# Kernel tuning notes

Measured on AMD Instinct MI355X. Metric: run time of the kernel, lower is better.

## Reference

```python
import jax, jax.numpy as jnp
import numpy as np

NEG_BIG = -9.0e15  # matches torch's -9000000000000000.0 mask fill
ALPHA = 0.2        # leakyrelu negative slope


def setup_inputs() -> dict:
    key = jax.random.key(0)
    k1, k2, k3, k4, k5 = jax.random.split(key, 5)
    N, F_in, F_out = 4096, 512, 64
    stdv = 1.0 / np.sqrt(F_out)
    x = jax.random.normal(k1, (N, F_in), dtype=jnp.float32)
    adj = jax.random.randint(k2, (N, N), 0, 2, dtype=jnp.int32)
    W = jax.random.uniform(k3, (F_in, F_out), dtype=jnp.float32, minval=-stdv, maxval=stdv)
    a = jax.random.normal(k4, (2 * F_out, 1), dtype=jnp.float32) * 0.1
    bias = jax.random.uniform(k5, (F_out,), dtype=jnp.float32, minval=-stdv, maxval=stdv)
    return {"x": x, "adj": adj, "W": W, "a": a, "bias": bias}


def _gat_forward(x, adj, W, a, bias):
    N = x.shape[0]
    F_out = W.shape[1]
    h = x @ W  # (N, F)
    a1 = a[:F_out, 0]   # weights hitting the first concat half
    a2 = a[F_out:, 0]   # weights hitting the second concat half
    # First half: row k=i*N+j of the concat holds h_j  ->  e1[j] = h_j . a1
    e1 = h @ a1  # (N,)
    # Second half of this repo's concat is NOT h_i; exact index algebra:
    # second[k=i*N+j, r] = h[(r*N+i)//F, (((r*N+i)%F)*N + j) % F]
    # Since it depends on j only via j % F, build table T[i, t] (t = j % F).
    r = jnp.arange(F_out)[:, None]          # (F, 1)
    i = jnp.arange(N)[None, :]              # (1, N)
    m = r * N + i                           # (F, N)
    p = m // F_out                          # row index into h
    s0 = m % F_out
    t = jnp.arange(F_out)                   # (F,)
    col = (s0[..., None] * N + t) % F_out   # (F, N, F) column index into h
    vals = h[p[..., None], col]             # (F, N, F)
    T = jnp.einsum('r,rit->it', a2, vals)   # (N, F)
    j = jnp.arange(N)
    e2 = T[:, j % F_out]                    # (N, N) second-half contribution
    e = e1[None, :] + e2                    # (N, N) pre-activation scores
    e = jnp.where(e > 0, e, ALPHA * e)      # LeakyReLU(0.2)
    e = jnp.where(adj > 0, e, NEG_BIG)      # mask non-edges
    att = jax.nn.softmax(e, axis=1)         # row-wise softmax (dropout = eval identity)
    out = jax.nn.relu(att @ h) + bias       # relu BEFORE bias add, as in source
    return out


def reference(x, adj, W, a, bias):
    return _gat_forward(x, adj, W, a, bias)
```

## Files before the change

kernel.cpp:

```cpp
#include <hip/hip_runtime.h>
#include <math.h>

#define N_NODES 4096
#define F_IN    512
#define F_OUT   64
#define ALPHA   0.2f

typedef _Float16 half8 __attribute__((ext_vector_type(8)));
typedef _Float16 half4 __attribute__((ext_vector_type(4)));
typedef float    floatx4 __attribute__((ext_vector_type(4)));

__global__ __launch_bounds__(256) void k_prep(const float* __restrict__ W,
                                              _Float16* __restrict__ WT) {
    int idx = blockIdx.x * 256 + threadIdx.x;
    int t = idx >> 9;
    int k = idx & 511;
    WT[idx] = (_Float16)W[k * F_OUT + t];
}

__global__ __launch_bounds__(256) void k_hW(const float* __restrict__ x,
                                            const _Float16* __restrict__ WT,
                                            const float* __restrict__ a,
                                            float* __restrict__ h,
                                            _Float16* __restrict__ hT,
                                            float* __restrict__ e1) {
    __shared__ float red[4][16][64];
    int tid  = threadIdx.x;
    int lane = tid & 63;
    int w    = tid >> 6;
    int i0   = blockIdx.x * 16;
    int n    = lane & 15;
    int quad = lane >> 4;

    floatx4 acc[4] = {{0,0,0,0},{0,0,0,0},{0,0,0,0},{0,0,0,0}};

    const float* xr = x + (size_t)(i0 + n) * F_IN + w * 128 + quad * 8;
    const _Float16* wb = WT + w * 128 + quad * 8;
#pragma unroll
    for (int kk = 0; kk < 128; kk += 32) {
        float4 x0 = *(const float4*)(xr + kk);
        float4 x1 = *(const float4*)(xr + kk + 4);
        half8 af = {(_Float16)x0.x, (_Float16)x0.y, (_Float16)x0.z, (_Float16)x0.w,
                    (_Float16)x1.x, (_Float16)x1.y, (_Float16)x1.z, (_Float16)x1.w};
#pragma unroll
        for (int g = 0; g < 4; ++g) {
            half8 bf = *(const half8*)(wb + (size_t)(g * 16 + n) * F_IN + kk);
            acc[g] = __builtin_amdgcn_mfma_f32_16x16x32_f16(af, bf, acc[g], 0, 0, 0);
        }
    }
#pragma unroll
    for (int g = 0; g < 4; ++g)
#pragma unroll
        for (int r = 0; r < 4; ++r)
            red[w][g * 4 + r][lane] = acc[g][r];
    __syncthreads();
    if (w != 0) return;
#pragma unroll
    for (int g = 0; g < 4; ++g)
#pragma unroll
        for (int r = 0; r < 4; ++r)
            acc[g][r] = red[0][g * 4 + r][lane] + red[1][g * 4 + r][lane] +
                        red[2][g * 4 + r][lane] + red[3][g * 4 + r][lane];
#pragma unroll
    for (int g = 0; g < 4; ++g) {
        half4 hv;
#pragma unroll
        for (int r = 0; r < 4; ++r) {
            h[(size_t)(i0 + quad * 4 + r) * F_OUT + g * 16 + n] = acc[g][r];
            hv[r] = (_Float16)acc[g][r];
        }
        *(half4*)(hT + (size_t)(g * 16 + n) * N_NODES + i0 + quad * 4) = hv;
    }
    float a1v[4];
#pragma unroll
    for (int g = 0; g < 4; ++g) a1v[g] = a[g * 16 + n];
#pragma unroll
    for (int r = 0; r < 4; ++r) {
        float v = acc[0][r] * a1v[0] + acc[1][r] * a1v[1] + acc[2][r] * a1v[2] + acc[3][r] * a1v[3];
        v += __shfl_xor(v, 1, 64);
        v += __shfl_xor(v, 2, 64);
        v += __shfl_xor(v, 4, 64);
        v += __shfl_xor(v, 8, 64);
        if (n == 0) e1[i0 + quad * 4 + r] = v;
    }
}

__global__ __launch_bounds__(256) void k_TqP(const float* __restrict__ h,
                                             const float* __restrict__ a,
                                             const float* __restrict__ e1,
                                             _Float16* __restrict__ P,
                                             float* __restrict__ out_pre,
                                             float* __restrict__ den) {
    __shared__ float part[4][64];
    __shared__ float TqS[64];
    int q = blockIdx.x;
    int tid = threadIdx.x;
    int t = tid & 63;
    int rp = tid >> 6;
    const float* a2 = a + F_OUT;
    float s = 0.f;
#pragma unroll
    for (int rr = 0; rr < 16; ++rr) {
        int r = rp * 16 + rr;
        s += a2[r] * h[(size_t)(r * 64 + q) * F_OUT + t];
    }
    part[rp][t] = s;
    float4 z = {0.f, 0.f, 0.f, 0.f};
#pragma unroll
    for (int it = 0; it < 4; ++it)
        ((float4*)out_pre)[(it * 64 + q) * 256 + tid] = z;
    if (tid < 16) ((float4*)den)[q * 16 + tid] = z;
    __syncthreads();
    if (tid < 64) TqS[tid] = part[0][tid] + part[1][tid] + part[2][tid] + part[3][tid];
    __syncthreads();
#pragma unroll
    for (int it = 0; it < 4; ++it) {
        int j = (it * 256 + tid) * 4;
        float4 ev = *(const float4*)(e1 + j);
        float4 tv = *(const float4*)(TqS + (j & 63));
        float e[4] = {ev.x + tv.x, ev.y + tv.y, ev.z + tv.z, ev.w + tv.w};
        half4 pv;
#pragma unroll
        for (int r = 0; r < 4; ++r) {
            float xx = e[r] > 0.f ? e[r] : ALPHA * e[r];
            pv[r] = (_Float16)__expf(xx);
        }
        *(half4*)(P + (size_t)q * N_NODES + j) = pv;
    }
}

__global__ __launch_bounds__(256, 4) void k_main(const int* __restrict__ adj,
                                                 const _Float16* __restrict__ P,
                                                 const _Float16* __restrict__ hT,
                                                 float* __restrict__ out_pre,
                                                 float* __restrict__ den) {
    int tid  = threadIdx.x;
    int lane = tid & 63;
    int w    = tid >> 6;
    int waveId = blockIdx.x * 4 + w;
    int g   = waveId >> 4;
    int s   = waveId & 15;
    int i0  = g * 16;
    int q   = i0 >> 6;
    int n    = lane & 15;
    int quad = lane >> 4;
    int jbase = s * 256 + quad * 8;

    const int*      arow = adj + (size_t)(i0 + n) * N_NODES + jbase;
    const _Float16* prow = P + (size_t)q * N_NODES + jbase;
    const _Float16* hrow = hT + (size_t)n * N_NODES + jbase;

    int4 abuf[16];
#pragma unroll
    for (int c = 0; c < 8; ++c) {
        abuf[2 * c]     = *(const int4*)(arow + c * 32);
        abuf[2 * c + 1] = *(const int4*)(arow + c * 32 + 4);
    }

    floatx4 acc[4] = {{0,0,0,0},{0,0,0,0},{0,0,0,0},{0,0,0,0}};
    floatx4 accd = {0, 0, 0, 0};
    _Float16 one_h = (n == 0) ? (_Float16)1.0f : (_Float16)0.0f;
    half8 ones_f = {one_h, one_h, one_h, one_h, one_h, one_h, one_h, one_h};

#pragma unroll
    for (int c = 0; c < 8; ++c) {
        int joff = c * 32;
        int4 a0 = abuf[2 * c];
        int4 a1v = abuf[2 * c + 1];
        half8 pv = *(const half8*)(prow + joff);
        half8 af;
        af[0] = a0.x  > 0 ? pv[0] : (_Float16)0.f;
        af[1] = a0.y  > 0 ? pv[1] : (_Float16)0.f;
        af[2] = a0.z  > 0 ? pv[2] : (_Float16)0.f;
        af[3] = a0.w  > 0 ? pv[3] : (_Float16)0.f;
        af[4] = a1v.x > 0 ? pv[4] : (_Float16)0.f;
        af[5] = a1v.y > 0 ? pv[5] : (_Float16)0.f;
        af[6] = a1v.z > 0 ? pv[6] : (_Float16)0.f;
        af[7] = a1v.w > 0 ? pv[7] : (_Float16)0.f;
#pragma unroll
        for (int g4 = 0; g4 < 4; ++g4) {
            half8 bf = *(const half8*)(hrow + (size_t)g4 * 16 * N_NODES + joff);
            acc[g4] = __builtin_amdgcn_mfma_f32_16x16x32_f16(af, bf, acc[g4], 0, 0, 0);
        }
        accd = __builtin_amdgcn_mfma_f32_16x16x32_f16(af, ones_f, accd, 0, 0, 0);
    }
#pragma unroll
    for (int gg = 0; gg < 4; ++gg) {
        int g4 = (gg + s) & 3;
#pragma unroll
        for (int rr = 0; rr < 4; ++rr) {
            int r = (rr + (s >> 2)) & 3;
            atomicAdd(&out_pre[(size_t)(i0 + quad * 4 + r) * F_OUT + g4 * 16 + n], acc[g4][r]);
        }
    }
    if (n == 0) {
#pragma unroll
        for (int r = 0; r < 4; ++r)
            atomicAdd(&den[i0 + quad * 4 + r], accd[r]);
    }
}

__global__ __launch_bounds__(256) void k_out(const float* __restrict__ out_pre,
                                             const float* __restrict__ den,
                                             const float* __restrict__ bias,
                                             float* __restrict__ out) {
    int idx = blockIdx.x * 256 + threadIdx.x;
    int i = idx >> 6;
    int t = idx & 63;
    float v = out_pre[idx] / den[i];
    v = v > 0.f ? v : 0.f;
    out[idx] = v + bias[t];
}

extern "C" void kernel_launch(void* const* d_in, const int* in_sizes, int n_in,
                              void* d_out, int out_size, void* d_ws, size_t ws_size,
                              hipStream_t stream) {
    const float* x    = (const float*)d_in[0];
    const int*   adj  = (const int*)d_in[1];
    const float* W    = (const float*)d_in[2];
    const float* a    = (const float*)d_in[3];
    const float* bias = (const float*)d_in[4];
    float* out = (float*)d_out;

    char* ws = (char*)d_ws;
    float*    h       = (float*)ws;
    _Float16* hT      = (_Float16*)(ws + 1024 * 1024);
    float*    e1      = (float*)(ws + 1536 * 1024);
    _Float16* P       = (_Float16*)(ws + 1552 * 1024);
    _Float16* WT      = (_Float16*)(ws + 2064 * 1024);
    float*    out_pre = (float*)(ws + 2128 * 1024);
    float*    den     = (float*)(ws + 3152 * 1024);

    k_prep<<<128, 256, 0, stream>>>(W, WT);
    k_hW  <<<256, 256, 0, stream>>>(x, WT, a, h, hT, e1);
    k_TqP <<<64, 256, 0, stream>>>(h, a, e1, P, out_pre, den);
    k_main<<<1024, 256, 0, stream>>>(adj, P, hT, out_pre, den);
    k_out <<<1024, 256, 0, stream>>>(out_pre, den, bias, out);
}
```

Before: 141.7 us.

## Replace atomic accumulation with per-split partial buffers reduced in output kernel

k_main now writes each j-split's partial output and denominator to separate buffers instead of using atomicAdd into a shared accumulator. k_out sums the 16 partials before normalising, so zero-initialising in k_TqP is no longer needed. A scheduling barrier is added after the adjacency prefetch. This trades atomic contention for a large partial buffer (16 MB) that must be written and read back.

New measurement: 139.1 us. About the same (-1.9%).

```diff
diff --git a/kernel.cpp b/kernel.cpp
--- a/kernel.cpp
+++ b/kernel.cpp
@@ -5,6 +5,7 @@
 #define F_IN    512
 #define F_OUT   64
 #define ALPHA   0.2f
+#define NPART   16
 
 typedef _Float16 half8 __attribute__((ext_vector_type(8)));
 typedef _Float16 half4 __attribute__((ext_vector_type(4)));
@@ -88,9 +89,7 @@
 __global__ __launch_bounds__(256) void k_TqP(const float* __restrict__ h,
                                              const float* __restrict__ a,
                                              const float* __restrict__ e1,
-                                             _Float16* __restrict__ P,
-                                             float* __restrict__ out_pre,
-                                             float* __restrict__ den) {
+                                             _Float16* __restrict__ P) {
     __shared__ float part[4][64];
     __shared__ float TqS[64];
     int q = blockIdx.x;
@@ -105,11 +104,6 @@
         s += a2[r] * h[(size_t)(r * 64 + q) * F_OUT + t];
     }
     part[rp][t] = s;
-    float4 z = {0.f, 0.f, 0.f, 0.f};
-#pragma unroll
-    for (int it = 0; it < 4; ++it)
-        ((float4*)out_pre)[(it * 64 + q) * 256 + tid] = z;
-    if (tid < 16) ((float4*)den)[q * 16 + tid] = z;
     __syncthreads();
     if (tid < 64) TqS[tid] = part[0][tid] + part[1][tid] + part[2][tid] + part[3][tid];
     __syncthreads();
@@ -132,8 +126,8 @@
 __global__ __launch_bounds__(256, 4) void k_main(const int* __restrict__ adj,
                                                  const _Float16* __restrict__ P,
                                                  const _Float16* __restrict__ hT,
-                                                 float* __restrict__ out_pre,
-                                                 float* __restrict__ den) {
+                                                 float* __restrict__ out_part,
+                                                 float* __restrict__ den_part) {
     int tid  = threadIdx.x;
     int lane = tid & 63;
     int w    = tid >> 6;
@@ -156,6 +150,7 @@
         abuf[2 * c]     = *(const int4*)(arow + c * 32);
         abuf[2 * c + 1] = *(const int4*)(arow + c * 32 + 4);
     }
+    __builtin_amdgcn_sched_barrier(0);
 
     floatx4 acc[4] = {{0,0,0,0},{0,0,0,0},{0,0,0,0},{0,0,0,0}};
     floatx4 accd = {0, 0, 0, 0};
@@ -184,30 +179,34 @@
         }
         accd = __builtin_amdgcn_mfma_f32_16x16x32_f16(af, ones_f, accd, 0, 0, 0);
     }
-#pragma unroll
-    for (int gg = 0; gg < 4; ++gg) {
-        int g4 = (gg + s) & 3;
-#pragma unroll
-        for (int rr = 0; rr < 4; ++rr) {
-            int r = (rr + (s >> 2)) & 3;
-            atomicAdd(&out_pre[(size_t)(i0 + quad * 4 + r) * F_OUT + g4 * 16 + n], acc[g4][r]);
-        }
-    }
+    float* op = out_part + ((size_t)s * N_NODES + i0) * F_OUT;
+#pragma unroll
+    for (int g4 = 0; g4 < 4; ++g4)
+#pragma unroll
+        for (int r = 0; r < 4; ++r)
+            op[(quad * 4 + r) * F_OUT + g4 * 16 + n] = acc[g4][r];
     if (n == 0) {
 #pragma unroll
         for (int r = 0; r < 4; ++r)
-            atomicAdd(&den[i0 + quad * 4 + r], accd[r]);
-    }
-}
-
-__global__ __launch_bounds__(256) void k_out(const float* __restrict__ out_pre,
-                                             const float* __restrict__ den,
+            den_part[s * N_NODES + i0 + quad * 4 + r] = accd[r];
+    }
+}
+
+__global__ __launch_bounds__(256) void k_out(const float* __restrict__ out_part,
+                                             const float* __restrict__ den_part,
                                              const float* __restrict__ bias,
                                              float* __restrict__ out) {
     int idx = blockIdx.x * 256 + threadIdx.x;
     int i = idx >> 6;
     int t = idx & 63;
-    float v = out_pre[idx] / den[i];
+    float sacc = 0.f, dacc = 0.f;
+#pragma unroll
+    for (int p = 0; p < NPART; ++p)
+        sacc += out_part[(size_t)p * N_NODES * F_OUT + idx];
+#pragma unroll
+    for (int p = 0; p < NPART; ++p)
+        dacc += den_part[p * N_NODES + i];
+    float v = sacc / dacc;
     v = v > 0.f ? v : 0.f;
     out[idx] = v + bias[t];
 }
@@ -223,17 +222,17 @@
     float* out = (float*)d_out;
 
     char* ws = (char*)d_ws;
-    float*    h       = (float*)ws;
-    _Float16* hT      = (_Float16*)(ws + 1024 * 1024);
-    float*    e1      = (float*)(ws + 1536 * 1024);
-    _Float16* P       = (_Float16*)(ws + 1552 * 1024);
-    _Float16* WT      = (_Float16*)(ws + 2064 * 1024);
-    float*    out_pre = (float*)(ws + 2128 * 1024);
-    float*    den     = (float*)(ws + 3152 * 1024);
+    float*    h        = (float*)ws;
+    _Float16* hT       = (_Float16*)(ws + 1024 * 1024);
+    float*    e1       = (float*)(ws + 1536 * 1024);
+    _Float16* P        = (_Float16*)(ws + 1552 * 1024);
+    _Float16* WT       = (_Float16*)(ws + 2064 * 1024);
+    float*    out_part = (float*)(ws + 2128 * 1024);
+    float*    den_part = (float*)(ws + (2128 + 16384) * 1024);
 
     k_prep<<<128, 256, 0, stream>>>(W, WT);
     k_hW  <<<256, 256, 0, stream>>>(x, WT, a, h, hT, e1);
-    k_TqP <<<64, 256, 0, stream>>>(h, a, e1, P, out_pre, den);
-    k_main<<<1024, 256, 0, stream>>>(adj, P, hT, out_pre, den);
-    k_out <<<1024, 256, 0, stream>>>(out_pre, den, bias, out);
-}
+    k_TqP <<<64, 256, 0, stream>>>(h, a, e1, P);
+    k_main<<<1024, 256, 0, stream>>>(adj, P, hT, out_part, den_part);
+    k_out <<<1024, 256, 0, stream>>>(out_part, den_part, bias, out);
+}
```
